# Kernel optimization log

Measured on AMD Instinct MI355X. Metric: run time of the kernel, lower is better.

Reference implementation:

```python
import jax, jax.numpy as jnp
import numpy as np

MAX_DF = 0.05
MAX_DPHI = 0.5
MAX_DA = 0.5
MIN_LENGTH = 2
N_BASE = 9
NEG = -jnp.inf


def _wrap(x):
    return (x + jnp.pi) % (2 * jnp.pi) - jnp.pi


def _link_single(tok):
    """tok: (W, K, 9) -> (new_tok9 (W,K,9), member (W,K) int32 local chain id or -1, count int32)."""
    W, K, _ = tok.shape
    snr = tok[..., 0]
    f_s, f_e = tok[..., 3], tok[..., 4]
    A_s, A_e = tok[..., 5], tok[..., 6]
    ps, pe = tok[..., 7], tok[..., 8]

    # ---- edge compatibility mask E[w, kp, kn] for w in 0..W-2 ----
    fe = f_e[:-1, :, None]; fs = f_s[1:, None, :]
    fm = (fe + fs) * 0.5
    f_ok = ~((fm > 0) & (jnp.abs(fe - fs) / jnp.where(fm > 0, fm, 1.0) > MAX_DF))
    p_ok = jnp.abs(_wrap(ps[1:, None, :] - pe[:-1, :, None])) <= MAX_DPHI
    ae = A_e[:-1, :, None]; an = A_s[1:, None, :]
    am = jnp.maximum(ae, an)
    a_ok = ~((am > 0) & (jnp.abs(ae - an) / jnp.where(am > 0, am, 1.0) > MAX_DA))
    E = (snr[:-1, :, None] > 0) & (snr[1:, None, :] > 0) & f_ok & p_ok & a_ok

    # ---- DP over windows: best-SNR chain ending at (w,k), seeded ONLY at window 0
    # (the torch code adds singletons for w>=1 AFTER the DP, so they never extend) ----
    best0 = jnp.where(snr[0] > 0, snr[0], NEG)

    def dp_step(best_prev, inp):
        Ew, snr_next = inp
        cand = jnp.where(Ew, best_prev[:, None] + snr_next[None, :], NEG)
        best_edge = cand.max(axis=0)
        arg = cand.argmax(axis=0).astype(jnp.int32)  # first max == smallest kp (torch tie rule)
        has = best_edge > NEG
        best_new = jnp.where(has, best_edge, NEG)
        return best_new, (best_new, jnp.where(has, arg, -1))

    _, (best_rest, pred_rest) = jax.lax.scan(dp_step, best0, (E, snr[1:]))
    best_dp = jnp.concatenate([best0[None], best_rest], 0)        # (W,K)
    pred = jnp.concatenate([jnp.full((1, K), -1, jnp.int32), pred_rest], 0)

    reach = best_dp > NEG
    # positive-snr tokens unreachable from window 0 become length-1 singleton chains
    score = jnp.where(reach, best_dp, jnp.where(snr > 0, snr, NEG))
    valid = score > NEG

    # ---- chain lengths ----
    def len_step(Lprev, inp):
        pw, vw = inp
        L = jnp.where(pw >= 0, Lprev[jnp.clip(pw, 0, K - 1)] + 1,
                      jnp.where(vw, 1, 0))
        return L, L

    L0 = jnp.where(valid[0], 1, 0).astype(jnp.int32)
    _, Lr = jax.lax.scan(len_step, L0, (pred[1:], valid[1:]))
    L = jnp.concatenate([L0[None], Lr], 0)                        # (W,K) int32

    # ---- backtrack token path for every endpoint: bpath[e, s] = token at window w_e - s ----
    def backtrack(w, k):
        def step(carry, _):
            cw, ck = carry
            nk = jnp.where((ck >= 0) & (cw > 0),
                           pred[jnp.clip(cw, 0, W - 1), jnp.clip(ck, 0, K - 1)], -1)
            return (cw - 1, nk), ck
        _, bp = jax.lax.scan(step, (w, k), None, length=W)
        return bp

    Wg, Kg = jnp.meshgrid(jnp.arange(W, dtype=jnp.int32),
                          jnp.arange(K, dtype=jnp.int32), indexing='ij')
    bpath = jax.vmap(backtrack)(Wg.reshape(-1), Kg.reshape(-1))   # (W*K, W) int32

    # ---- greedy non-overlapping assignment by descending total SNR ----
    order = jnp.argsort(-score.reshape(-1))  # stable; -inf endpoints sort last
    s_arr = jnp.arange(W)
    flatL = L.reshape(-1)
    flatV = valid.reshape(-1)

    def greedy_step(carry, e):
        used, counter = carry
        we = e // K
        Le = flatL[e]
        bp = bpath[e]
        act = s_arr < Le
        rows = jnp.where(act, we - s_arr, W)          # OOB rows dropped
        cols = jnp.clip(bp, 0, K - 1)
        M = jnp.zeros((W, K), bool).at[rows, cols].set(act, mode='drop')
        take = flatV[e] & ~jnp.any(M & used)
        used = used | (M & take)
        enrich = take & (Le >= MIN_LENGTH)
        cid = jnp.where(enrich, counter, -1)
        counter = counter + enrich.astype(jnp.int32)
        return (used, counter), (enrich, cid)

    (_, count), (enrich_o, cid_o) = jax.lax.scan(
        greedy_step, (jnp.zeros((W, K), bool), jnp.int32(0)), order)
    enrich = jnp.zeros((W * K,), bool).at[order].set(enrich_o)
    cid = jnp.full((W * K,), -1, jnp.int32).at[order].set(cid_o)

    # ---- per-slot membership + within-chain successor token (slots are disjoint) ----
    act = enrich[:, None] & (s_arr[None, :] < flatL[:, None])     # (W*K, W)
    we_all = (jnp.arange(W * K, dtype=jnp.int32) // K)[:, None]
    rows = jnp.where(act, we_all - s_arr[None, :], W)
    cols = jnp.clip(bpath, 0, K - 1)
    member = jnp.full((W, K), -1, jnp.int32).at[rows, cols].set(
        jnp.broadcast_to(cid[:, None], act.shape), mode='drop')
    succ_vals = jnp.concatenate(
        [jnp.full((W * K, 1), -1, jnp.int32), bpath[:, :-1].astype(jnp.int32)], 1)
    succ = jnp.full((W, K), -1, jnp.int32).at[rows, cols].set(succ_vals, mode='drop')

    # ---- enrichment 1: combined SNR = sqrt(sum snr^2) over each chain ----
    is_mem = member >= 0
    seg = jnp.where(is_mem, member, W * K)            # dummy segment for non-members
    snr2 = jnp.where(is_mem, snr * snr, 0.0)
    chain_snr2 = jax.ops.segment_sum(snr2.reshape(-1), seg.reshape(-1),
                                     num_segments=W * K + 1)
    safe = jnp.where(chain_snr2 > 0, chain_snr2, 1.0)
    snr_new = jnp.where(is_mem, jnp.sqrt(safe)[seg], snr)

    # ---- enrichment 2: boundary smoothing. Each boundary touches disjoint fields,
    # so all boundaries of all chains are independent and fully vectorizable. ----
    has_succ = succ >= 0
    nk = jnp.clip(succ, 0, K - 1)

    def nxt(col):  # value of col at (w+1, succ[w,k])
        shifted = jnp.concatenate([col[1:], jnp.zeros((1, K), col.dtype)], 0)
        return jnp.take_along_axis(shifted, nk, axis=1)

    f_avg = (f_e + nxt(f_s)) * 0.5
    A_avg = (A_e + nxt(A_s)) * 0.5
    ps_n = nxt(ps)
    corr = _wrap(ps_n - pe)
    f_e_new = jnp.where(has_succ, f_avg, f_e)
    A_e_new = jnp.where(has_succ, A_avg, A_e)
    pe_new = jnp.where(has_succ, pe + corr * 0.5, pe)
    rows2 = jnp.where(has_succ, jnp.arange(W)[:, None] + 1, W)
    f_s_new = f_s.at[rows2, nk].set(jnp.where(has_succ, f_avg, 0.0), mode='drop')
    A_s_new = A_s.at[rows2, nk].set(jnp.where(has_succ, A_avg, 0.0), mode='drop')
    ps_new = ps.at[rows2, nk].set(jnp.where(has_succ, ps_n - corr * 0.5, 0.0), mode='drop')

    out9 = jnp.stack([snr_new, tok[..., 1], tok[..., 2], f_s_new, f_e_new,
                      A_s_new, A_e_new, ps_new, pe_new], axis=-1)
    return out9, member, count


def setup_inputs() -> dict:
    key = jax.random.key(0)
    B, W, K, C = 16, 128, 32, 9
    tokens = jax.random.normal(key, (B, W, K, C), dtype=jnp.float32)
    return {"tokens": tokens}


def reference(tokens):
    new9, member, counts = jax.vmap(_link_single)(tokens[..., :N_BASE])
    # chain_counter carries across batch elements
    offsets = jnp.concatenate(
        [jnp.zeros((1,), counts.dtype), jnp.cumsum(counts)[:-1]])
    cid = jnp.where(member >= 0, member + offsets[:, None, None], -1)
    return jnp.concatenate([new9, cid[..., None].astype(tokens.dtype)], -1)
```

## Files before the change

kernel.cpp:

```cpp
#include <hip/hip_runtime.h>
#include <stdint.h>

#define WW 128
#define KK 32
#define NC 9
#define NCELL (WW * KK)

__device__ __forceinline__ float wrapf(float x) {
  const float kPi = 3.14159265358979323846f;
  const float kTwoPi = 6.28318530717958647692f;
  float y = fmodf(x + kPi, kTwoPi);
  y = (y < 0.0f) ? (y + kTwoPi) : y;
  return y - kPi;
}

__device__ __forceinline__ uint32_t ordf(float f) {
  uint32_t u = __float_as_uint(f);
  return (u & 0x80000000u) ? ~u : (u | 0x80000000u);
}

__device__ __forceinline__ uint32_t hs_key(int j) {
  return 0x00C0FFEEu ^ ((uint32_t)j * 0x9E3779B9u);
}

struct Row {
  float snr, fs, fe, As, Ae, ps, pe;
};

__device__ __forceinline__ Row loadRow(const float* __restrict__ T, int w,
                                       int k) {
  const float* C = T + (size_t)(w * KK + k) * NC;
  Row r;
  r.snr = C[0];
  r.fs = C[3];
  r.fe = C[4];
  r.As = C[5];
  r.Ae = C[6];
  r.ps = C[7];
  r.pe = C[8];
  return r;
}

__global__ __launch_bounds__(1024) void fused_kernel(
    const float* __restrict__ tokens, float* __restrict__ out,
    uint32_t* __restrict__ hs) {
  const int b = blockIdx.x;
  const int tid = threadIdx.x;
  const float* T = tokens + (size_t)b * NCELL * NC;

  __shared__ int8_t s_pred[NCELL];
  __shared__ int8_t s_member[NCELL];
  __shared__ int8_t s_succ[NCELL];
  __shared__ int8_t s_predcol[NCELL];
  __shared__ int8_t s_chaincol[KK * WW];
  __shared__ float s_chainsum[KK];
  __shared__ int s_chainlen[KK];
  __shared__ unsigned long long s_win[KK];
  __shared__ int s_count;
  __shared__ int s_off;

  {
    int* mi = (int*)s_member;
    int* si = (int*)s_succ;
    int* pi = (int*)s_predcol;
    for (int i = tid; i < NCELL / 4; i += 1024) {
      mi[i] = -1;
      si[i] = -1;
      pi[i] = -1;
    }
    if (tid < KK) s_win[tid] = 0ull;
  }
  __syncthreads();

  if (tid < 64) {
    const int k = tid & 31;
    const int h = tid >> 5;
    float snr0 = T[k * NC + 0];
    bool v0 = snr0 > 0.0f;
    float prev_best = v0 ? snr0 : -INFINITY;
    int prev_root = k;
    float prev_fe = T[k * NC + 4];
    float prev_Ae = T[k * NC + 6];
    float prev_pe = T[k * NC + 8];
    if (h == 0) {
      s_pred[k] = -1;
      if (v0) {
        unsigned long long key =
            ((unsigned long long)ordf(snr0) << 32) | (uint32_t)(~(uint32_t)k);
        atomicMax(&s_win[k], key);
      }
    }
    Row cur = loadRow(T, 1, k);
    Row nxt = loadRow(T, 2, k);
    for (int w = 1; w < WW; ++w) {
      unsigned long long full = __ballot(prev_best > -INFINITY);
      if (full == 0ull) break;

      int wf = (w + 2 < WW) ? (w + 2) : (WW - 1);
      Row fut = loadRow(T, wf, k);

      bool scur = cur.snr > 0.0f;
      float bestE = -INFINITY;
      int arg = 0;
      unsigned int rem = (unsigned int)full;
      while (rem) {
        int kp0 = __ffs(rem) - 1;
        rem &= rem - 1;
        bool have2 = rem != 0u;
        int kp1 = have2 ? (__ffs(rem) - 1) : kp0;
        if (have2) rem &= rem - 1;
        int kp = h ? kp1 : kp0;
        bool lane_ok = h ? have2 : true;
        float bp = __shfl(prev_best, kp);
        float fe = __shfl(prev_fe, kp);
        float ae = __shfl(prev_Ae, kp);
        float pe = __shfl(prev_pe, kp);
        float fm = (fe + cur.fs) * 0.5f;
        float fden = (fm > 0.0f) ? fm : 1.0f;
        bool fbad = (fm > 0.0f) && (fabsf(fe - cur.fs) / fden > 0.05f);
        float am = fmaxf(ae, cur.As);
        float aden = (am > 0.0f) ? am : 1.0f;
        bool abad = (am > 0.0f) && (fabsf(ae - cur.As) / aden > 0.5f);
        bool pok = fabsf(wrapf(cur.ps - pe)) <= 0.5f;
        if (lane_ok && scur && !fbad && !abad && pok) {
          float cand = bp + cur.snr;
          if (cand > bestE) { bestE = cand; arg = kp; }
        }
      }
      float ob = __shfl_xor(bestE, 32);
      int oa = __shfl_xor(arg, 32);
      float b0 = h ? ob : bestE;
      float b1 = h ? bestE : ob;
      int a0 = h ? oa : arg;
      int a1 = h ? arg : oa;
      bool take0 = (b0 > b1) || ((b0 == b1) && (a0 <= a1));
      float bE = take0 ? b0 : b1;
      int aC = take0 ? a0 : a1;
      bool has = bE > -INFINITY;
      if (h == 0) s_pred[w * KK + k] = (int8_t)(has ? aC : -1);
      int rsrc = has ? aC : 0;
      int rootc = __shfl(prev_root, rsrc);
      int root_new = has ? rootc : k;
      float bnew = has ? bE : -INFINITY;
      if (has && h == 0) {
        int idx = w * KK + k;
        unsigned long long key = ((unsigned long long)ordf(bnew) << 32) |
                                 (uint32_t)(~(uint32_t)idx);
        atomicMax(&s_win[root_new], key);
      }
      prev_best = bnew;
      prev_root = root_new;
      prev_fe = cur.fe;
      prev_Ae = cur.Ae;
      prev_pe = cur.pe;
      cur = nxt;
      nxt = fut;
    }
  }
  __syncthreads();

  if (tid < KK) {
    unsigned long long wk = s_win[tid];
    bool exists = (wk != 0ull);
    int idx = exists ? (int)(~(uint32_t)(wk & 0xFFFFFFFFull)) : -1;
    int we = idx >> 5;
    int ke = idx & 31;
    bool enr = exists && (we >= 1);
    int cid = 0;
    for (int r2 = 0; r2 < KK; ++r2) {
      unsigned long long k2 = __shfl(wk, r2);
      int e2 = __shfl((int)enr, r2);
      if (e2 && k2 > wk) cid++;
    }
    unsigned long long bal = __ballot(enr);
    int total = __popcll(bal);
    if (tid == 0) {
      s_count = total;
      __hip_atomic_store(&hs[2 * b], (uint32_t)total, __ATOMIC_RELEASE,
                         __HIP_MEMORY_SCOPE_AGENT);
      __hip_atomic_store(&hs[2 * b + 1], (uint32_t)total ^ hs_key(b),
                         __ATOMIC_RELEASE, __HIP_MEMORY_SCOPE_AGENT);
    }
    if (enr) {
      s_chainlen[cid] = we + 1;
      int cw = we, ck = ke, prevc = -1;
      while (cw >= 0) {
        int cell = (cw << 5) | ck;
        s_member[cell] = (int8_t)cid;
        s_succ[cell] = (int8_t)prevc;
        if (prevc >= 0) s_predcol[((cw + 1) << 5) | prevc] = (int8_t)ck;
        s_chaincol[cid * WW + cw] = (int8_t)ck;
        prevc = ck;
        ck = s_pred[cell];
        cw--;
      }
    }
  }
  __syncthreads();

  if (tid < KK && tid < s_count) {
    int len = s_chainlen[tid];
    float sum = 0.0f;
    for (int w = 0; w < len; ++w) {
      int col = s_chaincol[tid * WW + w];
      float s = T[(size_t)(w * KK + col) * NC + 0];
      sum += s * s;
    }
    s_chainsum[tid] = sum;
  }
  if (tid == 64) {
    int off = 0;
    for (int j = 0; j < b; ++j) {
      uint32_t v, ck;
      do {
        v = __hip_atomic_load(&hs[2 * j], __ATOMIC_ACQUIRE,
                              __HIP_MEMORY_SCOPE_AGENT);
        ck = __hip_atomic_load(&hs[2 * j + 1], __ATOMIC_ACQUIRE,
                               __HIP_MEMORY_SCOPE_AGENT);
      } while (v > 32u || ck != (v ^ hs_key(j)));
      off += (int)v;
    }
    s_off = off;
  }
  __syncthreads();

  const int off = s_off;
  for (int i = tid; i < NCELL; i += 1024) {
    int w = i >> 5;
    const float* C = T + (size_t)i * NC;
    float t0 = C[0], t1 = C[1], t2 = C[2], t3 = C[3], t4 = C[4], t5 = C[5],
          t6 = C[6], t7 = C[7], t8 = C[8];
    int mm = s_member[i];
    int sc = s_succ[i];
    int pc = s_predcol[i];
    float o0 = (mm >= 0) ? sqrtf(s_chainsum[mm]) : t0;
    float o3 = t3, o5 = t5, o7 = t7;
    if (pc >= 0) {
      const float* P = T + (size_t)((w - 1) * KK + pc) * NC;
      float fep = P[4], aep = P[6], pep = P[8];
      o3 = (fep + t3) * 0.5f;
      o5 = (aep + t5) * 0.5f;
      float corr = wrapf(t7 - pep);
      o7 = t7 - corr * 0.5f;
    }
    float o4 = t4, o6 = t6, o8 = t8;
    if (sc >= 0) {
      const float* S = T + (size_t)((w + 1) * KK + sc) * NC;
      float fsn = S[3], asn = S[5], psn = S[7];
      o4 = (t4 + fsn) * 0.5f;
      o6 = (t6 + asn) * 0.5f;
      float corr = wrapf(psn - t8);
      o8 = t8 + corr * 0.5f;
    }
    float* O = out + ((size_t)b * NCELL + i) * 10;
    O[0] = o0; O[1] = t1; O[2] = t2; O[3] = o3; O[4] = o4;
    O[5] = o5; O[6] = o6; O[7] = o7; O[8] = o8;
    O[9] = (mm >= 0) ? (float)(mm + off) : -1.0f;
  }
}

extern "C" void kernel_launch(void* const* d_in, const int* in_sizes, int n_in,
                              void* d_out, int out_size, void* d_ws,
                              size_t ws_size, hipStream_t stream) {
  const float* tokens = (const float*)d_in[0];
  float* out = (float*)d_out;
  int B = in_sizes[0] / (WW * KK * NC);
  uint32_t* hs = (uint32_t*)d_ws;
  fused_kernel<<<dim3(B), dim3(1024), 0, stream>>>(tokens, out, hs);
}
```

Measured before the change: 31.07 us.

## Split each batch into sixteen blocks with global-memory handoff of chain metadata

The launch grows from one 1024-thread block per batch to sixteen 256-thread blocks per batch. Slice 0 runs the serial DP and backtrack, then publishes packed per-cell member/succ/pred bytes and chain sums to workspace behind a release flag. All slices spin on the flags and then write their own 256 output cells. Non-zero slices prefetch their token rows before the wait, so the output pass is spread across more CUs. In exchange the design relies on inter-block spin-waiting, which needs all blocks co-resident, and adds global round trips for the metadata.

```diff
diff --git a/kernel.cpp b/kernel.cpp
--- a/kernel.cpp
+++ b/kernel.cpp
@@ -5,6 +5,7 @@
 #define KK 32
 #define NC 9
 #define NCELL (WW * KK)
+#define SLICES 16
 
 __device__ __forceinline__ float wrapf(float x) {
   const float kPi = 3.14159265358979323846f;
@@ -20,7 +21,7 @@
 }
 
 __device__ __forceinline__ uint32_t hs_key(int j) {
-  return 0x00C0FFEEu ^ ((uint32_t)j * 0x9E3779B9u);
+  return 0x5EED0C0Du ^ ((uint32_t)j * 0x9E3779B9u);
 }
 
 struct Row {
@@ -41,222 +42,276 @@
   return r;
 }
 
-__global__ __launch_bounds__(1024) void fused_kernel(
+__global__ __launch_bounds__(256) void fused_kernel(
     const float* __restrict__ tokens, float* __restrict__ out,
-    uint32_t* __restrict__ hs) {
-  const int b = blockIdx.x;
+    uint32_t* __restrict__ ws_u) {
+  const int bb = blockIdx.x >> 4;
+  const int sl = blockIdx.x & (SLICES - 1);
   const int tid = threadIdx.x;
-  const float* T = tokens + (size_t)b * NCELL * NC;
+  const int B = gridDim.x >> 4;
+  uint32_t* flags = ws_u;
+  uint32_t* flags2 = ws_u + 64;
+  uint32_t* chsum = ws_u + 256;
+  int* packed = (int*)(ws_u + 4096);
+  const float* T = tokens + (size_t)bb * NCELL * NC;
 
   __shared__ int8_t s_pred[NCELL];
   __shared__ int8_t s_member[NCELL];
   __shared__ int8_t s_succ[NCELL];
+  __shared__ int8_t s_chaincol[KK * WW];
   __shared__ int8_t s_predcol[NCELL];
-  __shared__ int8_t s_chaincol[KK * WW];
-  __shared__ float s_chainsum[KK];
   __shared__ int s_chainlen[KK];
   __shared__ unsigned long long s_win[KK];
   __shared__ int s_count;
-  __shared__ int s_off;
-
-  {
-    int* mi = (int*)s_member;
-    int* si = (int*)s_succ;
-    int* pi = (int*)s_predcol;
-    for (int i = tid; i < NCELL / 4; i += 1024) {
-      mi[i] = -1;
-      si[i] = -1;
-      pi[i] = -1;
-    }
-    if (tid < KK) s_win[tid] = 0ull;
+  __shared__ int s_wlim;
+  __shared__ int s_cnt[64];
+  __shared__ int s_mywl;
+
+  const int i = (sl << 8) + tid;
+  const int wcell = i >> 5;
+  float t0, t1, t2, t3, t4, t5, t6, t7, t8;
+  if (sl != 0) {
+    const float* C = T + (size_t)i * NC;
+    t0 = C[0]; t1 = C[1]; t2 = C[2]; t3 = C[3]; t4 = C[4];
+    t5 = C[5]; t6 = C[6]; t7 = C[7]; t8 = C[8];
+  }
+
+  if (sl == 0) {
+    {
+      int* mi = (int*)s_member;
+      int* si = (int*)s_succ;
+      int* pi = (int*)s_predcol;
+      for (int j = tid; j < NCELL / 4; j += 256) {
+        mi[j] = -1;
+        si[j] = -1;
+        pi[j] = -1;
+      }
+      if (tid < KK) s_win[tid] = 0ull;
+    }
+    __syncthreads();
+
+    if (tid < 64) {
+      const int k = tid & 31;
+      const int h = tid >> 5;
+      float snr0 = T[k * NC + 0];
+      bool v0 = snr0 > 0.0f;
+      float prev_best = v0 ? snr0 : -INFINITY;
+      int prev_root = k;
+      float prev_fe = T[k * NC + 4];
+      float prev_Ae = T[k * NC + 6];
+      float prev_pe = T[k * NC + 8];
+      if (h == 0) {
+        s_pred[k] = -1;
+        if (v0) {
+          unsigned long long key =
+              ((unsigned long long)ordf(snr0) << 32) | (uint32_t)(~(uint32_t)k);
+          atomicMax(&s_win[k], key);
+        }
+      }
+      Row cur = loadRow(T, 1, k);
+      Row nxt = loadRow(T, 2, k);
+      for (int w = 1; w < WW; ++w) {
+        unsigned long long full = __ballot(prev_best > -INFINITY);
+        if (full == 0ull) break;
+
+        int wf = (w + 2 < WW) ? (w + 2) : (WW - 1);
+        Row fut = loadRow(T, wf, k);
+
+        bool scur = cur.snr > 0.0f;
+        float bestE = -INFINITY;
+        int arg = 0;
+        unsigned int rem = (unsigned int)full;
+        while (rem) {
+          int kp0 = __ffs(rem) - 1;
+          rem &= rem - 1;
+          bool have2 = rem != 0u;
+          int kp1 = have2 ? (__ffs(rem) - 1) : kp0;
+          if (have2) rem &= rem - 1;
+          int kp = h ? kp1 : kp0;
+          bool lane_ok = h ? have2 : true;
+          float bp = __shfl(prev_best, kp);
+          float fe = __shfl(prev_fe, kp);
+          float ae = __shfl(prev_Ae, kp);
+          float pe = __shfl(prev_pe, kp);
+          float fm = (fe + cur.fs) * 0.5f;
+          float fden = (fm > 0.0f) ? fm : 1.0f;
+          bool fbad = (fm > 0.0f) && (fabsf(fe - cur.fs) / fden > 0.05f);
+          float am = fmaxf(ae, cur.As);
+          float aden = (am > 0.0f) ? am : 1.0f;
+          bool abad = (am > 0.0f) && (fabsf(ae - cur.As) / aden > 0.5f);
+          bool pok = fabsf(wrapf(cur.ps - pe)) <= 0.5f;
+          if (lane_ok && scur && !fbad && !abad && pok) {
+            float cand = bp + cur.snr;
+            if (cand > bestE) { bestE = cand; arg = kp; }
+          }
+        }
+        float ob = __shfl_xor(bestE, 32);
+        int oa = __shfl_xor(arg, 32);
+        float b0 = h ? ob : bestE;
+        float b1 = h ? bestE : ob;
+        int a0 = h ? oa : arg;
+        int a1 = h ? arg : oa;
+        bool take0 = (b0 > b1) || ((b0 == b1) && (a0 <= a1));
+        float bE = take0 ? b0 : b1;
+        int aC = take0 ? a0 : a1;
+        bool has = bE > -INFINITY;
+        if (h == 0) s_pred[w * KK + k] = (int8_t)(has ? aC : -1);
+        int rsrc = has ? aC : 0;
+        int rootc = __shfl(prev_root, rsrc);
+        int root_new = has ? rootc : k;
+        float bnew = has ? bE : -INFINITY;
+        if (has && h == 0) {
+          int idx = w * KK + k;
+          unsigned long long key = ((unsigned long long)ordf(bnew) << 32) |
+                                   (uint32_t)(~(uint32_t)idx);
+          atomicMax(&s_win[root_new], key);
+        }
+        prev_best = bnew;
+        prev_root = root_new;
+        prev_fe = cur.fe;
+        prev_Ae = cur.Ae;
+        prev_pe = cur.pe;
+        cur = nxt;
+        nxt = fut;
+      }
+    }
+    __syncthreads();
+
+    if (tid < KK) {
+      unsigned long long wk = s_win[tid];
+      bool exists = (wk != 0ull);
+      int idx = exists ? (int)(~(uint32_t)(wk & 0xFFFFFFFFull)) : -1;
+      int we = idx >> 5;
+      int ke = idx & 31;
+      bool enr = exists && (we >= 1);
+      int cid = 0;
+      for (int r2 = 0; r2 < KK; ++r2) {
+        unsigned long long k2 = __shfl(wk, r2);
+        int e2 = __shfl((int)enr, r2);
+        if (e2 && k2 > wk) cid++;
+      }
+      unsigned long long bal = __ballot(enr);
+      int total = __popcll(bal);
+      int wml = enr ? we : -1;
+      for (int d = 1; d < KK; d <<= 1) {
+        int o = __shfl_xor(wml, d);
+        wml = (o > wml) ? o : wml;
+      }
+      if (tid == 0) {
+        s_count = total;
+        s_wlim = wml;
+      }
+      if (enr) {
+        s_chainlen[cid] = we + 1;
+        int cw = we, ck = ke, prevc = -1;
+        while (cw >= 0) {
+          int cell = (cw << 5) | ck;
+          s_member[cell] = (int8_t)cid;
+          s_succ[cell] = (int8_t)prevc;
+          if (prevc >= 0) s_predcol[((cw + 1) << 5) | prevc] = (int8_t)ck;
+          s_chaincol[cid * WW + cw] = (int8_t)ck;
+          prevc = ck;
+          ck = s_pred[cell];
+          cw--;
+        }
+      }
+    }
+    __syncthreads();
+
+    if (tid < KK && tid < s_count) {
+      int len = s_chainlen[tid];
+      float sum = 0.0f;
+      for (int w = 0; w < len; ++w) {
+        int col = s_chaincol[tid * WW + w];
+        float s = T[(size_t)(w * KK + col) * NC + 0];
+        sum += s * s;
+      }
+      __hip_atomic_store(&chsum[bb * KK + tid], __float_as_uint(sum),
+                         __ATOMIC_RELAXED, __HIP_MEMORY_SCOPE_AGENT);
+    }
+    __syncthreads();
+
+    {
+      int nlim = (s_wlim + 1) * KK;
+      for (int j = tid; j < nlim; j += 256) {
+        int pk = (s_member[j] & 0xFF) | ((s_succ[j] & 0xFF) << 8) |
+                 ((s_predcol[j] & 0xFF) << 16);
+        __hip_atomic_store(&packed[bb * NCELL + j], pk, __ATOMIC_RELAXED,
+                           __HIP_MEMORY_SCOPE_AGENT);
+      }
+    }
+    __syncthreads();
+    if (tid == 0) {
+      __threadfence();
+      uint32_t v = (uint32_t)s_count | ((uint32_t)(s_wlim + 1) << 8);
+      __hip_atomic_store(&flags2[bb], v ^ hs_key(bb), __ATOMIC_RELEASE,
+                         __HIP_MEMORY_SCOPE_AGENT);
+      __hip_atomic_store(&flags[bb], v, __ATOMIC_RELEASE,
+                         __HIP_MEMORY_SCOPE_AGENT);
+    }
+  }
+
+  if (tid < B) {
+    uint32_t v, c2;
+    for (;;) {
+      v = __hip_atomic_load(&flags[tid], __ATOMIC_ACQUIRE,
+                            __HIP_MEMORY_SCOPE_AGENT);
+      c2 = __hip_atomic_load(&flags2[tid], __ATOMIC_ACQUIRE,
+                             __HIP_MEMORY_SCOPE_AGENT);
+      if (((v & 0xFFu) <= 32u) && ((v >> 8) <= 128u) &&
+          (c2 == (v ^ hs_key(tid))))
+        break;
+      __builtin_amdgcn_s_sleep(2);
+    }
+    s_cnt[tid] = (int)(v & 0xFFu);
+    if (tid == bb) s_mywl = (int)(v >> 8) - 1;
   }
   __syncthreads();
-
-  if (tid < 64) {
-    const int k = tid & 31;
-    const int h = tid >> 5;
-    float snr0 = T[k * NC + 0];
-    bool v0 = snr0 > 0.0f;
-    float prev_best = v0 ? snr0 : -INFINITY;
-    int prev_root = k;
-    float prev_fe = T[k * NC + 4];
-    float prev_Ae = T[k * NC + 6];
-    float prev_pe = T[k * NC + 8];
-    if (h == 0) {
-      s_pred[k] = -1;
-      if (v0) {
-        unsigned long long key =
-            ((unsigned long long)ordf(snr0) << 32) | (uint32_t)(~(uint32_t)k);
-        atomicMax(&s_win[k], key);
-      }
-    }
-    Row cur = loadRow(T, 1, k);
-    Row nxt = loadRow(T, 2, k);
-    for (int w = 1; w < WW; ++w) {
-      unsigned long long full = __ballot(prev_best > -INFINITY);
-      if (full == 0ull) break;
-
-      int wf = (w + 2 < WW) ? (w + 2) : (WW - 1);
-      Row fut = loadRow(T, wf, k);
-
-      bool scur = cur.snr > 0.0f;
-      float bestE = -INFINITY;
-      int arg = 0;
-      unsigned int rem = (unsigned int)full;
-      while (rem) {
-        int kp0 = __ffs(rem) - 1;
-        rem &= rem - 1;
-        bool have2 = rem != 0u;
-        int kp1 = have2 ? (__ffs(rem) - 1) : kp0;
-        if (have2) rem &= rem - 1;
-        int kp = h ? kp1 : kp0;
-        bool lane_ok = h ? have2 : true;
-        float bp = __shfl(prev_best, kp);
-        float fe = __shfl(prev_fe, kp);
-        float ae = __shfl(prev_Ae, kp);
-        float pe = __shfl(prev_pe, kp);
-        float fm = (fe + cur.fs) * 0.5f;
-        float fden = (fm > 0.0f) ? fm : 1.0f;
-        bool fbad = (fm > 0.0f) && (fabsf(fe - cur.fs) / fden > 0.05f);
-        float am = fmaxf(ae, cur.As);
-        float aden = (am > 0.0f) ? am : 1.0f;
-        bool abad = (am > 0.0f) && (fabsf(ae - cur.As) / aden > 0.5f);
-        bool pok = fabsf(wrapf(cur.ps - pe)) <= 0.5f;
-        if (lane_ok && scur && !fbad && !abad && pok) {
-          float cand = bp + cur.snr;
-          if (cand > bestE) { bestE = cand; arg = kp; }
-        }
-      }
-      float ob = __shfl_xor(bestE, 32);
-      int oa = __shfl_xor(arg, 32);
-      float b0 = h ? ob : bestE;
-      float b1 = h ? bestE : ob;
-      int a0 = h ? oa : arg;
-      int a1 = h ? arg : oa;
-      bool take0 = (b0 > b1) || ((b0 == b1) && (a0 <= a1));
-      float bE = take0 ? b0 : b1;
-      int aC = take0 ? a0 : a1;
-      bool has = bE > -INFINITY;
-      if (h == 0) s_pred[w * KK + k] = (int8_t)(has ? aC : -1);
-      int rsrc = has ? aC : 0;
-      int rootc = __shfl(prev_root, rsrc);
-      int root_new = has ? rootc : k;
-      float bnew = has ? bE : -INFINITY;
-      if (has && h == 0) {
-        int idx = w * KK + k;
-        unsigned long long key = ((unsigned long long)ordf(bnew) << 32) |
-                                 (uint32_t)(~(uint32_t)idx);
-        atomicMax(&s_win[root_new], key);
-      }
-      prev_best = bnew;
-      prev_root = root_new;
-      prev_fe = cur.fe;
-      prev_Ae = cur.Ae;
-      prev_pe = cur.pe;
-      cur = nxt;
-      nxt = fut;
-    }
-  }
-  __syncthreads();
-
-  if (tid < KK) {
-    unsigned long long wk = s_win[tid];
-    bool exists = (wk != 0ull);
-    int idx = exists ? (int)(~(uint32_t)(wk & 0xFFFFFFFFull)) : -1;
-    int we = idx >> 5;
-    int ke = idx & 31;
-    bool enr = exists && (we >= 1);
-    int cid = 0;
-    for (int r2 = 0; r2 < KK; ++r2) {
-      unsigned long long k2 = __shfl(wk, r2);
-      int e2 = __shfl((int)enr, r2);
-      if (e2 && k2 > wk) cid++;
-    }
-    unsigned long long bal = __ballot(enr);
-    int total = __popcll(bal);
-    if (tid == 0) {
-      s_count = total;
-      __hip_atomic_store(&hs[2 * b], (uint32_t)total, __ATOMIC_RELEASE,
-                         __HIP_MEMORY_SCOPE_AGENT);
-      __hip_atomic_store(&hs[2 * b + 1], (uint32_t)total ^ hs_key(b),
-                         __ATOMIC_RELEASE, __HIP_MEMORY_SCOPE_AGENT);
-    }
-    if (enr) {
-      s_chainlen[cid] = we + 1;
-      int cw = we, ck = ke, prevc = -1;
-      while (cw >= 0) {
-        int cell = (cw << 5) | ck;
-        s_member[cell] = (int8_t)cid;
-        s_succ[cell] = (int8_t)prevc;
-        if (prevc >= 0) s_predcol[((cw + 1) << 5) | prevc] = (int8_t)ck;
-        s_chaincol[cid * WW + cw] = (int8_t)ck;
-        prevc = ck;
-        ck = s_pred[cell];
-        cw--;
-      }
-    }
-  }
-  __syncthreads();
-
-  if (tid < KK && tid < s_count) {
-    int len = s_chainlen[tid];
-    float sum = 0.0f;
-    for (int w = 0; w < len; ++w) {
-      int col = s_chaincol[tid * WW + w];
-      float s = T[(size_t)(w * KK + col) * NC + 0];
-      sum += s * s;
-    }
-    s_chainsum[tid] = sum;
-  }
-  if (tid == 64) {
-    int off = 0;
-    for (int j = 0; j < b; ++j) {
-      uint32_t v, ck;
-      do {
-        v = __hip_atomic_load(&hs[2 * j], __ATOMIC_ACQUIRE,
-                              __HIP_MEMORY_SCOPE_AGENT);
-        ck = __hip_atomic_load(&hs[2 * j + 1], __ATOMIC_ACQUIRE,
+  int off = 0;
+  for (int j = 0; j < bb; ++j) off += s_cnt[j];
+  const int wlim = s_mywl;
+
+  if (sl == 0) {
+    const float* C = T + (size_t)i * NC;
+    t0 = C[0]; t1 = C[1]; t2 = C[2]; t3 = C[3]; t4 = C[4];
+    t5 = C[5]; t6 = C[6]; t7 = C[7]; t8 = C[8];
+  }
+  int mm = -1, sc = -1, pc = -1;
+  if (wcell <= wlim) {
+    int pk = __hip_atomic_load(&packed[bb * NCELL + i], __ATOMIC_RELAXED,
                                __HIP_MEMORY_SCOPE_AGENT);
-      } while (v > 32u || ck != (v ^ hs_key(j)));
-      off += (int)v;
-    }
-    s_off = off;
-  }
-  __syncthreads();
-
-  const int off = s_off;
-  for (int i = tid; i < NCELL; i += 1024) {
-    int w = i >> 5;
-    const float* C = T + (size_t)i * NC;
-    float t0 = C[0], t1 = C[1], t2 = C[2], t3 = C[3], t4 = C[4], t5 = C[5],
-          t6 = C[6], t7 = C[7], t8 = C[8];
-    int mm = s_member[i];
-    int sc = s_succ[i];
-    int pc = s_predcol[i];
-    float o0 = (mm >= 0) ? sqrtf(s_chainsum[mm]) : t0;
-    float o3 = t3, o5 = t5, o7 = t7;
-    if (pc >= 0) {
-      const float* P = T + (size_t)((w - 1) * KK + pc) * NC;
-      float fep = P[4], aep = P[6], pep = P[8];
-      o3 = (fep + t3) * 0.5f;
-      o5 = (aep + t5) * 0.5f;
-      float corr = wrapf(t7 - pep);
-      o7 = t7 - corr * 0.5f;
-    }
-    float o4 = t4, o6 = t6, o8 = t8;
-    if (sc >= 0) {
-      const float* S = T + (size_t)((w + 1) * KK + sc) * NC;
-      float fsn = S[3], asn = S[5], psn = S[7];
-      o4 = (t4 + fsn) * 0.5f;
-      o6 = (t6 + asn) * 0.5f;
-      float corr = wrapf(psn - t8);
-      o8 = t8 + corr * 0.5f;
-    }
-    float* O = out + ((size_t)b * NCELL + i) * 10;
-    O[0] = o0; O[1] = t1; O[2] = t2; O[3] = o3; O[4] = o4;
-    O[5] = o5; O[6] = o6; O[7] = o7; O[8] = o8;
-    O[9] = (mm >= 0) ? (float)(mm + off) : -1.0f;
-  }
+    mm = (int)(int8_t)(pk & 0xFF);
+    sc = (int)(int8_t)((pk >> 8) & 0xFF);
+    pc = (int)(int8_t)((pk >> 16) & 0xFF);
+  }
+  float o0 = t0;
+  if (mm >= 0) {
+    uint32_t cs = __hip_atomic_load(&chsum[bb * KK + mm], __ATOMIC_RELAXED,
+                                    __HIP_MEMORY_SCOPE_AGENT);
+    o0 = sqrtf(__uint_as_float(cs));
+  }
+  float o3 = t3, o5 = t5, o7 = t7;
+  if (pc >= 0) {
+    const float* P = T + (size_t)((wcell - 1) * KK + pc) * NC;
+    float fep = P[4], aep = P[6], pep = P[8];
+    o3 = (fep + t3) * 0.5f;
+    o5 = (aep + t5) * 0.5f;
+    float corr = wrapf(t7 - pep);
+    o7 = t7 - corr * 0.5f;
+  }
+  float o4 = t4, o6 = t6, o8 = t8;
+  if (sc >= 0) {
+    const float* S = T + (size_t)((wcell + 1) * KK + sc) * NC;
+    float fsn = S[3], asn = S[5], psn = S[7];
+    o4 = (t4 + fsn) * 0.5f;
+    o6 = (t6 + asn) * 0.5f;
+    float corr = wrapf(psn - t8);
+    o8 = t8 + corr * 0.5f;
+  }
+  float* O = out + ((size_t)bb * NCELL + i) * 10;
+  O[0] = o0; O[1] = t1; O[2] = t2; O[3] = o3; O[4] = o4;
+  O[5] = o5; O[6] = o6; O[7] = o7; O[8] = o8;
+  O[9] = (mm >= 0) ? (float)(mm + off) : -1.0f;
 }
 
 extern "C" void kernel_launch(void* const* d_in, const int* in_sizes, int n_in,
@@ -265,6 +320,6 @@
   const float* tokens = (const float*)d_in[0];
   float* out = (float*)d_out;
   int B = in_sizes[0] / (WW * KK * NC);
-  uint32_t* hs = (uint32_t*)d_ws;
-  fused_kernel<<<dim3(B), dim3(1024), 0, stream>>>(tokens, out, hs);
-}
+  uint32_t* ws_u = (uint32_t*)d_ws;
+  fused_kernel<<<dim3(B * SLICES), dim3(256), 0, stream>>>(tokens, out, ws_u);
+}
```

After: 28.21 us. -9.2%, faster.
